# Kernel optimization log

Hardware: AMD Instinct MI355X
Metric: run time of the kernel (lower is better)

The kernel has to match this reference:

```python
import jax, jax.numpy as jnp
import numpy as np

LN_EPS = 1e-5
IMPACT_FACTOR = 0.01
IMPACT_DIM = 16


def _layernorm(x, g, b):
    m = x.mean(-1, keepdims=True)
    v = x.var(-1, keepdims=True)
    return (x - m) / jnp.sqrt(v + LN_EPS) * g + b


def setup_inputs() -> dict:
    T, S, H, C, I, B = 50, 100, 256, 100, IMPACT_DIM, 4096
    key = jax.random.key(0)
    ks = jax.random.split(key, 6)
    s0 = jax.random.uniform(ks[0], (B, S), dtype=jnp.float32)
    prices = jax.random.uniform(ks[1], (B, T, S), dtype=jnp.float32)
    # Per-timestep policy params (nn.init.normal_(std=1), biases 0, LayerNorm affine g=1, b=0)
    W1 = jax.random.normal(ks[2], (T, H, S), dtype=jnp.float32)
    W2 = jax.random.normal(ks[3], (T, H, H), dtype=jnp.float32)
    Wo = jax.random.normal(ks[4], (T, C, H), dtype=jnp.float32)
    b1 = jnp.zeros((T, H)); b2 = jnp.zeros((T, H)); bo = jnp.zeros((T, C))
    g1 = jnp.ones((T, H)); be1 = jnp.zeros((T, H))
    g2 = jnp.ones((T, H)); be2 = jnp.zeros((T, H))
    return {"s0": s0, "prices": prices, "W1": W1, "b1": b1, "g1": g1, "be1": be1,
            "W2": W2, "b2": b2, "g2": g2, "be2": be2, "Wo": Wo, "bo": bo}


def reference(s0, prices, W1, b1, g1, be1, W2, b2, g2, be2, Wo, bo):
    B, S = s0.shape
    T = prices.shape[1]
    I = IMPACT_DIM
    # A_mat = impact_factor * eye(S); B_mat, C_mat are zeros (as in the source).
    B_mat = jnp.zeros((S, I), dtype=s0.dtype)
    C_mat = jnp.zeros((I, I), dtype=s0.dtype)
    # xi_t ~ N(0,1) noise drawn each step in the source forward.
    noise = jax.random.normal(jax.random.key(1), (T, B, I), dtype=s0.dtype)

    def policy(p, s):
        w1, bb1, gg1, bbe1, w2, bb2, gg2, bbe2, wo, bbo = p
        x = jax.nn.relu(_layernorm(s @ w1.T + bb1, gg1, bbe1))
        x = jax.nn.relu(_layernorm(x @ w2.T + bb2, gg2, bbe2))
        return x @ wo.T + bbo

    def step(carry, inp):
        s, x, cost = carry
        p_t, params, nz = inp  # p_t: [B,S]
        a = jnp.minimum(policy(params, s), s)
        # P @ (A @ P @ a + B @ x) with A = f*I  ->  p * (f * p * a + x @ B^T)
        impact = p_t * (IMPACT_FACTOR * p_t * a + x @ B_mat.T)
        cost = cost + jnp.sum((p_t + impact) * a, axis=1)
        s = s - a
        x = x @ C_mat.T + nz
        return (s, x, cost), None

    prices_t = jnp.moveaxis(prices, 1, 0)  # [T,B,S]
    params_stack = (W1[:-1], b1[:-1], g1[:-1], be1[:-1],
                    W2[:-1], b2[:-1], g2[:-1], be2[:-1], Wo[:-1], bo[:-1])
    carry0 = (s0, jnp.zeros((B, I), dtype=s0.dtype), jnp.zeros((B,), dtype=s0.dtype))
    (s, x, cost), _ = jax.lax.scan(step, carry0, (prices_t[:-1], params_stack, noise[:-1]))
    # Final step t = T-1: a_t = s_t (liquidate remainder, no policy)
    p_T = prices_t[-1]
    a = s
    impact = p_T * (IMPACT_FACTOR * p_T * a + x @ B_mat.T)
    cost = cost + jnp.sum((p_T + impact) * a, axis=1)
    return cost.mean()
```

## Files before the change

kernel.cpp:

```cpp
#include <hip/hip_runtime.h>
#include <stdint.h>

#define TT 50
#define NSTEP 49
#define NBATCH 4096
#define SS 100
#define HH 256
#define K1 128
#define NO 128
#define MROWS 16
#define NBLK 256
#define NTHR 512

typedef short bf16x8 __attribute__((ext_vector_type(8)));
typedef float f32x4 __attribute__((ext_vector_type(4)));

#define MFMA(a, b, c) __builtin_amdgcn_mfma_f32_16x16x32_bf16((a), (b), (c), 0, 0, 0)

#define W1G_OFF(t, nt, ks) ((((size_t)(t) * 16 + (nt)) * 4 + (ks)) * 512)
#define W2G_OFF(t, nt, ks) ((((size_t)(t) * 16 + (nt)) * 8 + (ks)) * 512)
#define WOG_OFF(t, nt, ks) ((((size_t)(t) * 8 + (nt)) * 8 + (ks)) * 512)
#define N_W1G W1G_OFF(TT, 0, 0)
#define N_W2G W2G_OFF(TT, 0, 0)
#define N_WOG WOG_OFF(TT, 0, 0)

__device__ __forceinline__ void bar_lds() {
  __asm__ volatile("s_waitcnt lgkmcnt(0)\n\ts_barrier" ::: "memory");
}
__device__ __forceinline__ void pin_loads() { __builtin_amdgcn_sched_barrier(0); }

__device__ __forceinline__ short f2b(float f) {
  union { float f; uint32_t u; } v;
  v.f = f;
  return (short)((v.u + 0x7FFFu + ((v.u >> 16) & 1u)) >> 16);
}

__device__ __forceinline__ bf16x8 cvt8(const float* __restrict__ p) {
  bf16x8 r;
#pragma unroll
  for (int j = 0; j < 8; ++j) r[j] = f2b(p[j]);
  return r;
}

__device__ __forceinline__ bf16x8 ldpad(const float* __restrict__ rowp, int k, int kmax) {
  bf16x8 r;
#pragma unroll
  for (int j = 0; j < 8; ++j) {
    int kk = k + j;
    r[j] = (kk < kmax) ? f2b(rowp[kk]) : (short)0;
  }
  return r;
}

__global__ void zero_out(float* out) {
  if (threadIdx.x == 0 && blockIdx.x == 0) out[0] = 0.f;
}

__global__ __launch_bounds__(256) void prep(
    const float* __restrict__ W1, const float* __restrict__ b1,
    const float* __restrict__ W2, const float* __restrict__ Wo,
    short* __restrict__ W1g, short* __restrict__ W2g, short* __restrict__ Wog,
    float* __restrict__ out) {
  __shared__ float tile[16 * 264];
  const int tid = threadIdx.x;
  const int wg = blockIdx.x;
  if (wg == 0 && tid == 0) out[0] = 0.f;
  if (wg < 800) {
    const int t = wg >> 4, nt = wg & 15;
    const float* src = W1 + ((size_t)t * HH + nt * 16) * SS;
    const float* bsrc = b1 + t * HH + nt * 16;
    for (int i = tid; i < 16 * K1; i += 256) {
      int m = i >> 7, k = i & 127;
      float v = (k < SS) ? src[m * SS + k] : (k == SS ? bsrc[m] : 0.f);
      tile[m * 264 + k] = v;
    }
    __syncthreads();
    {
      int ks = tid >> 6, lane = tid & 63;
      int qq = lane >> 4, cc = lane & 15;
      bf16x8 v;
#pragma unroll
      for (int j = 0; j < 8; ++j) v[j] = f2b(tile[cc * 264 + ks * 32 + qq * 8 + j]);
      *(bf16x8*)&W1g[W1G_OFF(t, nt, ks) + lane * 8] = v;
    }
  } else if (wg < 1600) {
    const int h = wg - 800;
    const int t = h >> 4, nt = h & 15;
    const float* src = W2 + ((size_t)t * HH + nt * 16) * HH;
    for (int i = tid; i < 16 * HH; i += 256) {
      int m = i >> 8, k = i & 255;
      tile[m * 264 + k] = src[m * HH + k];
    }
    __syncthreads();
    for (int gi = tid; gi < 512; gi += 256) {
      int ks = gi >> 6, lane = gi & 63;
      int qq = lane >> 4, cc = lane & 15;
      bf16x8 v;
#pragma unroll
      for (int j = 0; j < 8; ++j) v[j] = f2b(tile[cc * 264 + ks * 32 + qq * 8 + j]);
      *(bf16x8*)&W2g[W2G_OFF(t, nt, ks) + lane * 8] = v;
    }
  } else {
    const int h = wg - 1600;
    const int t = h >> 3, nt = h & 7;
    for (int i = tid; i < 16 * HH; i += 256) {
      int m = i >> 8, k = i & 255;
      int n = nt * 16 + m;
      tile[m * 264 + k] = (n < SS) ? Wo[((size_t)t * SS + n) * HH + k] : 0.f;
    }
    __syncthreads();
    for (int gi = tid; gi < 512; gi += 256) {
      int ks = gi >> 6, lane = gi & 63;
      int qq = lane >> 4, cc = lane & 15;
      bf16x8 v;
#pragma unroll
      for (int j = 0; j < 8; ++j) v[j] = f2b(tile[cc * 264 + ks * 32 + qq * 8 + j]);
      *(bf16x8*)&Wog[WOG_OFF(t, nt, ks) + lane * 8] = v;
    }
  }
}

template <int MODE>
__global__ __launch_bounds__(NTHR, 2) void run_kernel(
    const float* __restrict__ s0, const float* __restrict__ prices,
    const float* __restrict__ b1, const float* __restrict__ g1, const float* __restrict__ be1,
    const float* __restrict__ b2, const float* __restrict__ g2, const float* __restrict__ be2,
    const float* __restrict__ bo,
    const float* __restrict__ W1f, const float* __restrict__ W2f, const float* __restrict__ Wof,
    const short* __restrict__ W1g, const short* __restrict__ W2g, const short* __restrict__ Wog,
    float* __restrict__ out) {
  __shared__ short sbuf[MROWS][K1 + 8];
  __shared__ short xb1[MROWS][HH + 8];
  __shared__ short xb2[MROWS][HH + 8];
  __shared__ float lnred[MROWS][17];
  __shared__ float wsum[8];

  const int tid = threadIdx.x;
  const int w = tid >> 6;
  const int lane = tid & 63;
  const int q = lane >> 4;
  const int c16 = lane & 15;
  const int b0 = blockIdx.x * MROWS;

  const int n0 = w * 32 + c16;
  const int n1 = n0 + 16;
  const int col = w * 16 + c16;
  const bool cvalid = col < SS;

  for (int j = tid; j < MROWS * (K1 + 8); j += NTHR) ((short*)sbuf)[j] = 0;
  __syncthreads();

  float s_reg[4];
#pragma unroll
  for (int r = 0; r < 4; ++r) {
    int row = q * 4 + r;
    s_reg[r] = cvalid ? s0[(size_t)(b0 + row) * SS + col] : 0.f;
    if (cvalid) sbuf[row][col] = f2b(s_reg[r]);
  }
  __syncthreads();

  bf16x8 w1f[8];
  auto loadW1 = [&](int t) {
#pragma unroll
    for (int ks = 0; ks < 4; ++ks) {
      if (MODE == 0) {
        w1f[2 * ks + 0] = *(const bf16x8*)&W1g[W1G_OFF(t, 2 * w, ks) + lane * 8];
        w1f[2 * ks + 1] = *(const bf16x8*)&W1g[W1G_OFF(t, 2 * w + 1, ks) + lane * 8];
      } else {
        const int k = ks * 32 + q * 8;
        w1f[2 * ks + 0] = ldpad(W1f + ((size_t)t * HH + n0) * SS, k, SS);
        w1f[2 * ks + 1] = ldpad(W1f + ((size_t)t * HH + n1) * SS, k, SS);
      }
    }
  };
  float pr[4];
  auto loadP = [&](int t) {
#pragma unroll
    for (int r = 0; r < 4; ++r) {
      int row = q * 4 + r;
      pr[r] = cvalid ? prices[((size_t)(b0 + row) * TT + t) * SS + col] : 0.f;
    }
  };

  auto ln_epi = [&](f32x4& a0, f32x4& a1, float bv0, float bv1, float gv0, float gv1,
                    float ev0, float ev1, short (*dst)[HH + 8]) {
    float p1[4], p2[4];
#pragma unroll
    for (int r = 0; r < 4; ++r) {
      float v0 = a0[r] + bv0;
      float v1 = a1[r] + bv1;
      a0[r] = v0;
      a1[r] = v1;
      p1[r] = v0 + v1;
      p2[r] = v0 * v0 + v1 * v1;
    }
#pragma unroll
    for (int m = 1; m <= 8; m <<= 1)
#pragma unroll
      for (int r = 0; r < 4; ++r) {
        p1[r] += __shfl_xor(p1[r], m);
        p2[r] += __shfl_xor(p2[r], m);
      }
    if (c16 == 0) {
#pragma unroll
      for (int r = 0; r < 4; ++r) {
        lnred[q * 4 + r][2 * w] = p1[r];
        lnred[q * 4 + r][2 * w + 1] = p2[r];
      }
    }
    bar_lds();
    float meanv = 0.f, rstdv = 0.f;
    if (lane < 16) {
      float S1 = 0.f, S2 = 0.f;
#pragma unroll
      for (int i = 0; i < 8; ++i) {
        S1 += lnred[lane][2 * i];
        S2 += lnred[lane][2 * i + 1];
      }
      meanv = S1 * (1.f / HH);
      float var = fmaxf(S2 * (1.f / HH) - meanv * meanv, 0.f);
      rstdv = rsqrtf(var + 1e-5f);
    }
#pragma unroll
    for (int r = 0; r < 4; ++r) {
      int row = q * 4 + r;
      float mean = __shfl(meanv, row);
      float rstd = __shfl(rstdv, row);
      float v0 = (a0[r] - mean) * rstd * gv0 + ev0;
      float v1 = (a1[r] - mean) * rstd * gv1 + ev1;
      dst[row][n0] = f2b(fmaxf(v0, 0.f));
      dst[row][n1] = f2b(fmaxf(v1, 0.f));
    }
    bar_lds();
  };

  loadW1(0);
  loadP(0);
  float costreg = 0.f;

#pragma unroll 1
  for (int t = 0; t < NSTEP; ++t) {
    const float b1v0 = b1[t * HH + n0], b1v1 = b1[t * HH + n1];
    const float g1v0 = g1[t * HH + n0], g1v1 = g1[t * HH + n1];
    const float e1v0 = be1[t * HH + n0], e1v1 = be1[t * HH + n1];
    const float b2v0 = b2[t * HH + n0], b2v1 = b2[t * HH + n1];
    const float g2v0 = g2[t * HH + n0], g2v1 = g2[t * HH + n1];
    const float e2v0 = be2[t * HH + n0], e2v1 = be2[t * HH + n1];
    const float bov = cvalid ? bo[t * SS + col] : 0.f;

    f32x4 acc0 = (f32x4){0.f, 0.f, 0.f, 0.f};
    f32x4 acc1 = (f32x4){0.f, 0.f, 0.f, 0.f};
#pragma unroll
    for (int ks = 0; ks < 4; ++ks) {
      bf16x8 a = *(const bf16x8*)&sbuf[c16][ks * 32 + q * 8];
      acc0 = MFMA(a, w1f[2 * ks + 0], acc0);
      acc1 = MFMA(a, w1f[2 * ks + 1], acc1);
    }

    bf16x8 w2f[16];
#pragma unroll
    for (int ks = 0; ks < 8; ++ks) {
      if (MODE == 0) {
        w2f[2 * ks + 0] = *(const bf16x8*)&W2g[W2G_OFF(t, 2 * w, ks) + lane * 8];
        w2f[2 * ks + 1] = *(const bf16x8*)&W2g[W2G_OFF(t, 2 * w + 1, ks) + lane * 8];
      } else {
        const int k = ks * 32 + q * 8;
        w2f[2 * ks + 0] = cvt8(W2f + ((size_t)t * HH + n0) * HH + k);
        w2f[2 * ks + 1] = cvt8(W2f + ((size_t)t * HH + n1) * HH + k);
      }
    }
    pin_loads();

    ln_epi(acc0, acc1, b1v0, b1v1, g1v0, g1v1, e1v0, e1v1, xb1);

    f32x4 acc0b = (f32x4){0.f, 0.f, 0.f, 0.f};
    f32x4 acc1b = (f32x4){0.f, 0.f, 0.f, 0.f};
    acc0 = (f32x4){0.f, 0.f, 0.f, 0.f};
    acc1 = (f32x4){0.f, 0.f, 0.f, 0.f};
#pragma unroll
    for (int ks = 0; ks < 4; ++ks) {
      bf16x8 a = *(const bf16x8*)&xb1[c16][ks * 32 + q * 8];
      acc0 = MFMA(a, w2f[2 * ks + 0], acc0);
      acc1 = MFMA(a, w2f[2 * ks + 1], acc1);
    }
#pragma unroll
    for (int ks = 4; ks < 8; ++ks) {
      bf16x8 a = *(const bf16x8*)&xb1[c16][ks * 32 + q * 8];
      acc0b = MFMA(a, w2f[2 * ks + 0], acc0b);
      acc1b = MFMA(a, w2f[2 * ks + 1], acc1b);
    }
    acc0 = acc0 + acc0b;
    acc1 = acc1 + acc1b;

    bf16x8 wof[8];
#pragma unroll
    for (int ks = 0; ks < 8; ++ks) {
      if (MODE == 0) {
        wof[ks] = *(const bf16x8*)&Wog[WOG_OFF(t, w, ks) + lane * 8];
      } else {
        const int k = ks * 32 + q * 8;
        if (cvalid) {
          wof[ks] = cvt8(Wof + ((size_t)t * SS + col) * HH + k);
        } else {
          bf16x8 z = {0, 0, 0, 0, 0, 0, 0, 0};
          wof[ks] = z;
        }
      }
    }
    pin_loads();

    ln_epi(acc0, acc1, b2v0, b2v1, g2v0, g2v1, e2v0, e2v1, xb2);

    f32x4 a3 = (f32x4){0.f, 0.f, 0.f, 0.f};
    f32x4 a3b = (f32x4){0.f, 0.f, 0.f, 0.f};
#pragma unroll
    for (int ks = 0; ks < 4; ++ks) {
      bf16x8 a = *(const bf16x8*)&xb2[c16][ks * 32 + q * 8];
      a3 = MFMA(a, wof[ks], a3);
    }
#pragma unroll
    for (int ks = 4; ks < 8; ++ks) {
      bf16x8 a = *(const bf16x8*)&xb2[c16][ks * 32 + q * 8];
      a3b = MFMA(a, wof[ks], a3b);
    }
    a3 = a3 + a3b;

    float pcur[4];
#pragma unroll
    for (int r = 0; r < 4; ++r) pcur[r] = pr[r];
    const int tn = (t + 1 < NSTEP) ? t + 1 : 0;
    loadW1(tn);
    loadP(t + 1);
    pin_loads();

#pragma unroll
    for (int r = 0; r < 4; ++r) {
      float o = a3[r] + bov;
      float a = fminf(o, s_reg[r]);
      float pa = pcur[r] * a;
      costreg += pa + 0.01f * pa * pa;
      s_reg[r] -= a;
      if (cvalid) sbuf[q * 4 + r][col] = f2b(s_reg[r]);
    }
    bar_lds();
  }

#pragma unroll
  for (int r = 0; r < 4; ++r) {
    float pa = pr[r] * s_reg[r];
    costreg += pa + 0.01f * pa * pa;
  }

#pragma unroll
  for (int m = 1; m < 64; m <<= 1) costreg += __shfl_xor(costreg, m);
  if (lane == 0) wsum[w] = costreg;
  __syncthreads();
  if (tid == 0) {
    float tot = 0.f;
#pragma unroll
    for (int i = 0; i < 8; ++i) tot += wsum[i];
    atomicAdd(out, tot * (1.f / NBATCH));
  }
}

extern "C" void kernel_launch(void* const* d_in, const int* in_sizes, int n_in,
                              void* d_out, int out_size, void* d_ws, size_t ws_size,
                              hipStream_t stream) {
  const float* s0 = (const float*)d_in[0];
  const float* prices = (const float*)d_in[1];
  const float* W1 = (const float*)d_in[2];
  const float* b1 = (const float*)d_in[3];
  const float* g1 = (const float*)d_in[4];
  const float* be1 = (const float*)d_in[5];
  const float* W2 = (const float*)d_in[6];
  const float* b2 = (const float*)d_in[7];
  const float* g2 = (const float*)d_in[8];
  const float* be2 = (const float*)d_in[9];
  const float* Wo = (const float*)d_in[10];
  const float* bo = (const float*)d_in[11];
  float* out = (float*)d_out;

  const size_t need = (N_W1G + N_W2G + N_WOG) * sizeof(short);

  if (ws_size >= need) {
    short* W1g = (short*)d_ws;
    short* W2g = W1g + N_W1G;
    short* Wog = W2g + N_W2G;
    prep<<<dim3(2000), dim3(256), 0, stream>>>(W1, b1, W2, Wo, W1g, W2g, Wog, out);
    run_kernel<0><<<dim3(NBLK), dim3(NTHR), 0, stream>>>(
        s0, prices, b1, g1, be1, b2, g2, be2, bo,
        W1, W2, Wo, W1g, W2g, Wog, out);
  } else {
    zero_out<<<dim3(1), dim3(64), 0, stream>>>(out);
    run_kernel<1><<<dim3(NBLK), dim3(NTHR), 0, stream>>>(
        s0, prices, b1, g1, be1, b2, g2, be2, bo,
        W1, W2, Wo, (const short*)nullptr, (const short*)nullptr, (const short*)nullptr, out);
  }
}
```

Baseline: 403.9 us.

## Stage W2 fragments through LDS via direct global-to-LDS loads

```diff
diff --git a/kernel.cpp b/kernel.cpp
--- a/kernel.cpp
+++ b/kernel.cpp
@@ -27,7 +27,9 @@
 __device__ __forceinline__ void bar_lds() {
   __asm__ volatile("s_waitcnt lgkmcnt(0)\n\ts_barrier" ::: "memory");
 }
-__device__ __forceinline__ void pin_loads() { __builtin_amdgcn_sched_barrier(0); }
+__device__ __forceinline__ void wait_vm0() {
+  __asm__ volatile("s_waitcnt vmcnt(0)" ::: "memory");
+}
 
 __device__ __forceinline__ short f2b(float f) {
   union { float f; uint32_t u; } v;
@@ -121,7 +123,7 @@
 }
 
 template <int MODE>
-__global__ __launch_bounds__(NTHR, 2) void run_kernel(
+__global__ __launch_bounds__(NTHR, 1) void run_kernel(
     const float* __restrict__ s0, const float* __restrict__ prices,
     const float* __restrict__ b1, const float* __restrict__ g1, const float* __restrict__ be1,
     const float* __restrict__ b2, const float* __restrict__ g2, const float* __restrict__ be2,
@@ -129,6 +131,7 @@
     const float* __restrict__ W1f, const float* __restrict__ W2f, const float* __restrict__ Wof,
     const short* __restrict__ W1g, const short* __restrict__ W2g, const short* __restrict__ Wog,
     float* __restrict__ out) {
+  __shared__ short w2s[8][16][512];
   __shared__ short sbuf[MROWS][K1 + 8];
   __shared__ short xb1[MROWS][HH + 8];
   __shared__ short xb2[MROWS][HH + 8];
@@ -257,22 +260,21 @@
       acc1 = MFMA(a, w1f[2 * ks + 1], acc1);
     }
 
-    bf16x8 w2f[16];
-#pragma unroll
-    for (int ks = 0; ks < 8; ++ks) {
-      if (MODE == 0) {
-        w2f[2 * ks + 0] = *(const bf16x8*)&W2g[W2G_OFF(t, 2 * w, ks) + lane * 8];
-        w2f[2 * ks + 1] = *(const bf16x8*)&W2g[W2G_OFF(t, 2 * w + 1, ks) + lane * 8];
-      } else {
-        const int k = ks * 32 + q * 8;
-        w2f[2 * ks + 0] = cvt8(W2f + ((size_t)t * HH + n0) * HH + k);
-        w2f[2 * ks + 1] = cvt8(W2f + ((size_t)t * HH + n1) * HH + k);
-      }
-    }
-    pin_loads();
+    if (MODE == 0) {
+#pragma unroll
+      for (int ks = 0; ks < 8; ++ks) {
+        __builtin_amdgcn_global_load_lds(
+            (const uint32_t*)&W2g[W2G_OFF(t, 2 * w, ks) + lane * 8],
+            (uint32_t*)&w2s[w][2 * ks][0], 16, 0, 0);
+        __builtin_amdgcn_global_load_lds(
+            (const uint32_t*)&W2g[W2G_OFF(t, 2 * w + 1, ks) + lane * 8],
+            (uint32_t*)&w2s[w][2 * ks + 1][0], 16, 0, 0);
+      }
+    }
 
     ln_epi(acc0, acc1, b1v0, b1v1, g1v0, g1v1, e1v0, e1v1, xb1);
 
+    if (MODE == 0) wait_vm0();
     f32x4 acc0b = (f32x4){0.f, 0.f, 0.f, 0.f};
     f32x4 acc1b = (f32x4){0.f, 0.f, 0.f, 0.f};
     acc0 = (f32x4){0.f, 0.f, 0.f, 0.f};
@@ -280,14 +282,32 @@
 #pragma unroll
     for (int ks = 0; ks < 4; ++ks) {
       bf16x8 a = *(const bf16x8*)&xb1[c16][ks * 32 + q * 8];
-      acc0 = MFMA(a, w2f[2 * ks + 0], acc0);
-      acc1 = MFMA(a, w2f[2 * ks + 1], acc1);
+      bf16x8 bA, bB;
+      if (MODE == 0) {
+        bA = *(const bf16x8*)&w2s[w][2 * ks + 0][lane * 8];
+        bB = *(const bf16x8*)&w2s[w][2 * ks + 1][lane * 8];
+      } else {
+        const int k = ks * 32 + q * 8;
+        bA = cvt8(W2f + ((size_t)t * HH + n0) * HH + k);
+        bB = cvt8(W2f + ((size_t)t * HH + n1) * HH + k);
+      }
+      acc0 = MFMA(a, bA, acc0);
+      acc1 = MFMA(a, bB, acc1);
     }
 #pragma unroll
     for (int ks = 4; ks < 8; ++ks) {
       bf16x8 a = *(const bf16x8*)&xb1[c16][ks * 32 + q * 8];
-      acc0b = MFMA(a, w2f[2 * ks + 0], acc0b);
-      acc1b = MFMA(a, w2f[2 * ks + 1], acc1b);
+      bf16x8 bA, bB;
+      if (MODE == 0) {
+        bA = *(const bf16x8*)&w2s[w][2 * ks + 0][lane * 8];
+        bB = *(const bf16x8*)&w2s[w][2 * ks + 1][lane * 8];
+      } else {
+        const int k = ks * 32 + q * 8;
+        bA = cvt8(W2f + ((size_t)t * HH + n0) * HH + k);
+        bB = cvt8(W2f + ((size_t)t * HH + n1) * HH + k);
+      }
+      acc0b = MFMA(a, bA, acc0b);
+      acc1b = MFMA(a, bB, acc1b);
     }
     acc0 = acc0 + acc0b;
     acc1 = acc1 + acc1b;
@@ -307,7 +327,6 @@
         }
       }
     }
-    pin_loads();
 
     ln_epi(acc0, acc1, b2v0, b2v1, g2v0, g2v1, e2v0, e2v1, xb2);
 
@@ -331,7 +350,6 @@
     const int tn = (t + 1 < NSTEP) ? t + 1 : 0;
     loadW1(tn);
     loadP(t + 1);
-    pin_loads();
 
 #pragma unroll
     for (int r = 0; r < 4; ++r) {
@@ -392,7 +410,7 @@
         W1, W2, Wo, W1g, W2g, Wog, out);
   } else {
     zero_out<<<dim3(1), dim3(64), 0, stream>>>(out);
-    run_kernel<1><<<dim3(NBLK), dim3(NTHR), 0, stream>>>(
+    run_kernel<1><<<dim3(256), dim3(NTHR), 0, stream>>>(
         s0, prices, b1, g1, be1, b2, g2, be2, bo,
         W1, W2, Wo, (const short*)nullptr, (const short*)nullptr, (const short*)nullptr, out);
   }
```

Measured after the change: 449.4 us. 1.11x slower.

## Double waves per block, one 16-col tile per wave, LDS-atomic LN stats

Applied to the files above, without the earlier changes.

```diff
diff --git a/kernel.cpp b/kernel.cpp
--- a/kernel.cpp
+++ b/kernel.cpp
@@ -7,13 +7,13 @@
 #define SS 100
 #define HH 256
 #define K1 128
-#define NO 128
 #define MROWS 16
 #define NBLK 256
-#define NTHR 512
+#define NTHR 1024
 
 typedef short bf16x8 __attribute__((ext_vector_type(8)));
 typedef float f32x4 __attribute__((ext_vector_type(4)));
+typedef float f32x2 __attribute__((ext_vector_type(2)));
 
 #define MFMA(a, b, c) __builtin_amdgcn_mfma_f32_16x16x32_bf16((a), (b), (c), 0, 0, 0)
 
@@ -27,7 +27,6 @@
 __device__ __forceinline__ void bar_lds() {
   __asm__ volatile("s_waitcnt lgkmcnt(0)\n\ts_barrier" ::: "memory");
 }
-__device__ __forceinline__ void pin_loads() { __builtin_amdgcn_sched_barrier(0); }
 
 __device__ __forceinline__ short f2b(float f) {
   union { float f; uint32_t u; } v;
@@ -121,7 +120,7 @@
 }
 
 template <int MODE>
-__global__ __launch_bounds__(NTHR, 2) void run_kernel(
+__global__ __launch_bounds__(NTHR, 4) void run_kernel(
     const float* __restrict__ s0, const float* __restrict__ prices,
     const float* __restrict__ b1, const float* __restrict__ g1, const float* __restrict__ be1,
     const float* __restrict__ b2, const float* __restrict__ g2, const float* __restrict__ be2,
@@ -132,8 +131,9 @@
   __shared__ short sbuf[MROWS][K1 + 8];
   __shared__ short xb1[MROWS][HH + 8];
   __shared__ short xb2[MROWS][HH + 8];
-  __shared__ float lnred[MROWS][17];
-  __shared__ float wsum[8];
+  __shared__ float st0[2][32];
+  __shared__ float st1[2][32];
+  __shared__ float wsum[16];
 
   const int tid = threadIdx.x;
   const int w = tid >> 6;
@@ -142,57 +142,46 @@
   const int c16 = lane & 15;
   const int b0 = blockIdx.x * MROWS;
 
-  const int n0 = w * 32 + c16;
-  const int n1 = n0 + 16;
-  const int col = w * 16 + c16;
-  const bool cvalid = col < SS;
+  const int n0 = w * 16 + c16;
+  const bool g3 = w < 8;
+  const int col3 = (w & 7) * 16 + c16;
+  const bool cvalid = g3 && (col3 < SS);
 
   for (int j = tid; j < MROWS * (K1 + 8); j += NTHR) ((short*)sbuf)[j] = 0;
+  if (tid < 64) {
+    ((float*)st0)[tid] = 0.f;
+    ((float*)st1)[tid] = 0.f;
+  }
   __syncthreads();
 
-  float s_reg[4];
+  float s_reg[4], pr[4];
 #pragma unroll
   for (int r = 0; r < 4; ++r) {
-    int row = q * 4 + r;
-    s_reg[r] = cvalid ? s0[(size_t)(b0 + row) * SS + col] : 0.f;
-    if (cvalid) sbuf[row][col] = f2b(s_reg[r]);
-  }
-  __syncthreads();
-
-  bf16x8 w1f[8];
-  auto loadW1 = [&](int t) {
-#pragma unroll
-    for (int ks = 0; ks < 4; ++ks) {
-      if (MODE == 0) {
-        w1f[2 * ks + 0] = *(const bf16x8*)&W1g[W1G_OFF(t, 2 * w, ks) + lane * 8];
-        w1f[2 * ks + 1] = *(const bf16x8*)&W1g[W1G_OFF(t, 2 * w + 1, ks) + lane * 8];
-      } else {
-        const int k = ks * 32 + q * 8;
-        w1f[2 * ks + 0] = ldpad(W1f + ((size_t)t * HH + n0) * SS, k, SS);
-        w1f[2 * ks + 1] = ldpad(W1f + ((size_t)t * HH + n1) * SS, k, SS);
-      }
-    }
-  };
-  float pr[4];
-  auto loadP = [&](int t) {
+    s_reg[r] = 0.f;
+    pr[r] = 0.f;
+  }
+  if (cvalid) {
 #pragma unroll
     for (int r = 0; r < 4; ++r) {
       int row = q * 4 + r;
-      pr[r] = cvalid ? prices[((size_t)(b0 + row) * TT + t) * SS + col] : 0.f;
-    }
-  };
-
-  auto ln_epi = [&](f32x4& a0, f32x4& a1, float bv0, float bv1, float gv0, float gv1,
-                    float ev0, float ev1, short (*dst)[HH + 8]) {
-    float p1[4], p2[4];
+      s_reg[r] = s0[(size_t)(b0 + row) * SS + col3];
+      pr[r] = prices[((size_t)(b0 + row) * TT) * SS + col3];
+      sbuf[row][col3] = f2b(s_reg[r]);
+    }
+  }
+  __syncthreads();
+
+  float costreg = 0.f;
+
+  auto ln_epi = [&](f32x4& acc, float bv, float gv, float ev,
+                    short (*dst)[HH + 8], float (*st)[32], int par) {
+    float hv[4], p1[4], p2[4];
 #pragma unroll
     for (int r = 0; r < 4; ++r) {
-      float v0 = a0[r] + bv0;
-      float v1 = a1[r] + bv1;
-      a0[r] = v0;
-      a1[r] = v1;
-      p1[r] = v0 + v1;
-      p2[r] = v0 * v0 + v1 * v1;
+      float v = acc[r] + bv;
+      hv[r] = v;
+      p1[r] = v;
+      p2[r] = v * v;
     }
 #pragma unroll
     for (int m = 1; m <= 8; m <<= 1)
@@ -204,143 +193,124 @@
     if (c16 == 0) {
 #pragma unroll
       for (int r = 0; r < 4; ++r) {
-        lnred[q * 4 + r][2 * w] = p1[r];
-        lnred[q * 4 + r][2 * w + 1] = p2[r];
+        atomicAdd(&st[par][(q * 4 + r) * 2 + 0], p1[r]);
+        atomicAdd(&st[par][(q * 4 + r) * 2 + 1], p2[r]);
       }
     }
     bar_lds();
-    float meanv = 0.f, rstdv = 0.f;
-    if (lane < 16) {
-      float S1 = 0.f, S2 = 0.f;
-#pragma unroll
-      for (int i = 0; i < 8; ++i) {
-        S1 += lnred[lane][2 * i];
-        S2 += lnred[lane][2 * i + 1];
-      }
-      meanv = S1 * (1.f / HH);
-      float var = fmaxf(S2 * (1.f / HH) - meanv * meanv, 0.f);
-      rstdv = rsqrtf(var + 1e-5f);
-    }
+    if (w == 0 && lane < 32) st[par ^ 1][lane] = 0.f;
 #pragma unroll
     for (int r = 0; r < 4; ++r) {
-      int row = q * 4 + r;
-      float mean = __shfl(meanv, row);
-      float rstd = __shfl(rstdv, row);
-      float v0 = (a0[r] - mean) * rstd * gv0 + ev0;
-      float v1 = (a1[r] - mean) * rstd * gv1 + ev1;
-      dst[row][n0] = f2b(fmaxf(v0, 0.f));
-      dst[row][n1] = f2b(fmaxf(v1, 0.f));
+      f32x2 sv = *(const f32x2*)&st[par][(q * 4 + r) * 2];
+      float mean = sv[0] * (1.f / HH);
+      float var = fmaxf(sv[1] * (1.f / HH) - mean * mean, 0.f);
+      float rstd = rsqrtf(var + 1e-5f);
+      float x = (hv[r] - mean) * rstd * gv + ev;
+      dst[q * 4 + r][n0] = f2b(fmaxf(x, 0.f));
     }
     bar_lds();
   };
 
-  loadW1(0);
-  loadP(0);
-  float costreg = 0.f;
-
 #pragma unroll 1
   for (int t = 0; t < NSTEP; ++t) {
-    const float b1v0 = b1[t * HH + n0], b1v1 = b1[t * HH + n1];
-    const float g1v0 = g1[t * HH + n0], g1v1 = g1[t * HH + n1];
-    const float e1v0 = be1[t * HH + n0], e1v1 = be1[t * HH + n1];
-    const float b2v0 = b2[t * HH + n0], b2v1 = b2[t * HH + n1];
-    const float g2v0 = g2[t * HH + n0], g2v1 = g2[t * HH + n1];
-    const float e2v0 = be2[t * HH + n0], e2v1 = be2[t * HH + n1];
-    const float bov = cvalid ? bo[t * SS + col] : 0.f;
-
-    f32x4 acc0 = (f32x4){0.f, 0.f, 0.f, 0.f};
-    f32x4 acc1 = (f32x4){0.f, 0.f, 0.f, 0.f};
+    const int par = t & 1;
+    const float b1v = b1[t * HH + n0], g1v = g1[t * HH + n0], e1v = be1[t * HH + n0];
+    const float b2v = b2[t * HH + n0], g2v = g2[t * HH + n0], e2v = be2[t * HH + n0];
+
+    bf16x8 w1f[4];
 #pragma unroll
     for (int ks = 0; ks < 4; ++ks) {
+      if (MODE == 0) {
+        w1f[ks] = *(const bf16x8*)&W1g[W1G_OFF(t, w, ks) + lane * 8];
+      } else {
+        w1f[ks] = ldpad(W1f + ((size_t)t * HH + n0) * SS, ks * 32 + q * 8, SS);
+      }
+    }
+    f32x4 acc = (f32x4){0.f, 0.f, 0.f, 0.f};
+    f32x4 accb = (f32x4){0.f, 0.f, 0.f, 0.f};
+#pragma unroll
+    for (int ks = 0; ks < 2; ++ks) {
       bf16x8 a = *(const bf16x8*)&sbuf[c16][ks * 32 + q * 8];
-      acc0 = MFMA(a, w1f[2 * ks + 0], acc0);
-      acc1 = MFMA(a, w1f[2 * ks + 1], acc1);
-    }
-
-    bf16x8 w2f[16];
+      acc = MFMA(a, w1f[ks], acc);
+    }
+#pragma unroll
+    for (int ks = 2; ks < 4; ++ks) {
+      bf16x8 a = *(const bf16x8*)&sbuf[c16][ks * 32 + q * 8];
+      accb = MFMA(a, w1f[ks], accb);
+    }
+    acc = acc + accb;
+
+    ln_epi(acc, b1v, g1v, e1v, xb1, st0, par);
+
+    bf16x8 w2f[8];
 #pragma unroll
     for (int ks = 0; ks < 8; ++ks) {
       if (MODE == 0) {
-        w2f[2 * ks + 0] = *(const bf16x8*)&W2g[W2G_OFF(t, 2 * w, ks) + lane * 8];
-        w2f[2 * ks + 1] = *(const bf16x8*)&W2g[W2G_OFF(t, 2 * w + 1, ks) + lane * 8];
+        w2f[ks] = *(const bf16x8*)&W2g[W2G_OFF(t, w, ks) + lane * 8];
       } else {
-        const int k = ks * 32 + q * 8;
-        w2f[2 * ks + 0] = cvt8(W2f + ((size_t)t * HH + n0) * HH + k);
-        w2f[2 * ks + 1] = cvt8(W2f + ((size_t)t * HH + n1) * HH + k);
-      }
-    }
-    pin_loads();
-
-    ln_epi(acc0, acc1, b1v0, b1v1, g1v0, g1v1, e1v0, e1v1, xb1);
-
-    f32x4 acc0b = (f32x4){0.f, 0.f, 0.f, 0.f};
-    f32x4 acc1b = (f32x4){0.f, 0.f, 0.f, 0.f};
-    acc0 = (f32x4){0.f, 0.f, 0.f, 0.f};
-    acc1 = (f32x4){0.f, 0.f, 0.f, 0.f};
+        w2f[ks] = cvt8(W2f + ((size_t)t * HH + n0) * HH + ks * 32 + q * 8);
+      }
+    }
+    acc = (f32x4){0.f, 0.f, 0.f, 0.f};
+    accb = (f32x4){0.f, 0.f, 0.f, 0.f};
 #pragma unroll
     for (int ks = 0; ks < 4; ++ks) {
       bf16x8 a = *(const bf16x8*)&xb1[c16][ks * 32 + q * 8];
-      acc0 = MFMA(a, w2f[2 * ks + 0], acc0);
-      acc1 = MFMA(a, w2f[2 * ks + 1], acc1);
+      acc = MFMA(a, w2f[ks], acc);
     }
 #pragma unroll
     for (int ks = 4; ks < 8; ++ks) {
       bf16x8 a = *(const bf16x8*)&xb1[c16][ks * 32 + q * 8];
-      acc0b = MFMA(a, w2f[2 * ks + 0], acc0b);
-      acc1b = MFMA(a, w2f[2 * ks + 1], acc1b);
-    }
-    acc0 = acc0 + acc0b;
-    acc1 = acc1 + acc1b;
-
-    bf16x8 wof[8];
-#pragma unroll
-    for (int ks = 0; ks < 8; ++ks) {
-      if (MODE == 0) {
-        wof[ks] = *(const bf16x8*)&Wog[WOG_OFF(t, w, ks) + lane * 8];
-      } else {
-        const int k = ks * 32 + q * 8;
-        if (cvalid) {
-          wof[ks] = cvt8(Wof + ((size_t)t * SS + col) * HH + k);
+      accb = MFMA(a, w2f[ks], accb);
+    }
+    acc = acc + accb;
+
+    ln_epi(acc, b2v, g2v, e2v, xb2, st1, par);
+
+    f32x4 a3 = (f32x4){0.f, 0.f, 0.f, 0.f};
+    if (g3) {
+      bf16x8 wof[8];
+#pragma unroll
+      for (int ks = 0; ks < 8; ++ks) {
+        if (MODE == 0) {
+          wof[ks] = *(const bf16x8*)&Wog[WOG_OFF(t, w & 7, ks) + lane * 8];
         } else {
-          bf16x8 z = {0, 0, 0, 0, 0, 0, 0, 0};
-          wof[ks] = z;
+          if (col3 < SS) {
+            wof[ks] = cvt8(Wof + ((size_t)t * SS + col3) * HH + ks * 32 + q * 8);
+          } else {
+            bf16x8 z = {0, 0, 0, 0, 0, 0, 0, 0};
+            wof[ks] = z;
+          }
         }
       }
-    }
-    pin_loads();
-
-    ln_epi(acc0, acc1, b2v0, b2v1, g2v0, g2v1, e2v0, e2v1, xb2);
-
-    f32x4 a3 = (f32x4){0.f, 0.f, 0.f, 0.f};
-    f32x4 a3b = (f32x4){0.f, 0.f, 0.f, 0.f};
-#pragma unroll
-    for (int ks = 0; ks < 4; ++ks) {
-      bf16x8 a = *(const bf16x8*)&xb2[c16][ks * 32 + q * 8];
-      a3 = MFMA(a, wof[ks], a3);
-    }
-#pragma unroll
-    for (int ks = 4; ks < 8; ++ks) {
-      bf16x8 a = *(const bf16x8*)&xb2[c16][ks * 32 + q * 8];
-      a3b = MFMA(a, wof[ks], a3b);
-    }
-    a3 = a3 + a3b;
-
-    float pcur[4];
-#pragma unroll
-    for (int r = 0; r < 4; ++r) pcur[r] = pr[r];
-    const int tn = (t + 1 < NSTEP) ? t + 1 : 0;
-    loadW1(tn);
-    loadP(t + 1);
-    pin_loads();
-
-#pragma unroll
-    for (int r = 0; r < 4; ++r) {
-      float o = a3[r] + bov;
-      float a = fminf(o, s_reg[r]);
-      float pa = pcur[r] * a;
-      costreg += pa + 0.01f * pa * pa;
-      s_reg[r] -= a;
-      if (cvalid) sbuf[q * 4 + r][col] = f2b(s_reg[r]);
+      f32x4 a3b = (f32x4){0.f, 0.f, 0.f, 0.f};
+#pragma unroll
+      for (int ks = 0; ks < 4; ++ks) {
+        bf16x8 a = *(const bf16x8*)&xb2[c16][ks * 32 + q * 8];
+        a3 = MFMA(a, wof[ks], a3);
+      }
+#pragma unroll
+      for (int ks = 4; ks < 8; ++ks) {
+        bf16x8 a = *(const bf16x8*)&xb2[c16][ks * 32 + q * 8];
+        a3b = MFMA(a, wof[ks], a3b);
+      }
+      a3 = a3 + a3b;
+    }
+
+    if (cvalid) {
+      const float bov = bo[t * SS + col3];
+#pragma unroll
+      for (int r = 0; r < 4; ++r) {
+        float o = a3[r] + bov;
+        float a = fminf(o, s_reg[r]);
+        float pa = pr[r] * a;
+        costreg += pa + 0.01f * pa * pa;
+        s_reg[r] -= a;
+        sbuf[q * 4 + r][col3] = f2b(s_reg[r]);
+      }
+#pragma unroll
+      for (int r = 0; r < 4; ++r)
+        pr[r] = prices[((size_t)(b0 + q * 4 + r) * TT + t + 1) * SS + col3];
     }
     bar_lds();
   }
@@ -350,7 +320,6 @@
     float pa = pr[r] * s_reg[r];
     costreg += pa + 0.01f * pa * pa;
   }
-
 #pragma unroll
   for (int m = 1; m < 64; m <<= 1) costreg += __shfl_xor(costreg, m);
   if (lane == 0) wsum[w] = costreg;
@@ -358,7 +327,7 @@
   if (tid == 0) {
     float tot = 0.f;
 #pragma unroll
-    for (int i = 0; i < 8; ++i) tot += wsum[i];
+    for (int i = 0; i < 16; ++i) tot += wsum[i];
     atomicAdd(out, tot * (1.f / NBATCH));
   }
 }
```

After: 518.8 us. 1.28x slower.
